# Optimization experiments

Measured on AMD Instinct MI355X. Metric: run time of the kernel, lower is better.

## Reference

```python
import jax, jax.numpy as jnp
import numpy as np

# ---- constants matching init_kwargs ----
ALPHA = 1.0
SCALING = 12.0
RESP_INDEX = (0, 1, 2, 3)
N_TARGETS = len(RESP_INDEX)
NDAYS = 250  # number of distinct date ids; with N=2M and 250 ids all are present
N = 2_000_000
N_RESP = 5


def setup_inputs() -> dict:
    key = jax.random.key(0)
    k1, k2, k3, k4 = jax.random.split(key, 4)
    inputs = jax.random.normal(k1, (N, N_RESP), dtype=jnp.float32)
    targets = jax.random.normal(k2, (N, N_RESP), dtype=jnp.float32)
    weights = jax.random.uniform(k3, (N,), dtype=jnp.float32)
    date = jax.random.randint(k4, (N,), 0, NDAYS, dtype=jnp.int64)
    return {"inputs": inputs, "targets": targets, "weights": weights, "date": date}


def reference(inputs, targets, weights, date):
    # slice resp columns (resp_index is not None and len < 5)
    idx = jnp.asarray(RESP_INDEX)
    x = jax.nn.sigmoid(SCALING * inputs[..., idx])   # [N, 4]
    t = targets[..., idx]                            # [N, 4]

    # faithful to torch: inputs/targets flattened sample-major, while
    # weights/date are repeat-tiled (resp-major) -- same pairing as original.
    x = x.reshape(-1)                 # [4N], sample-major
    t = t.reshape(-1)                 # [4N], sample-major
    w = jnp.tile(weights, N_TARGETS)  # [4N], tiled
    d = jnp.tile(date, N_TARGETS)     # [4N], tiled

    # per-day grouped sum -> single-pass segment reduction
    Pi = jax.ops.segment_sum(w * t * x, d, num_segments=NDAYS)  # [NDAYS]

    sumPi = Pi.sum()
    # normalize == 'mean'
    loss = -ALPHA * sumPi * jnp.maximum(sumPi, 0.0) / jnp.sum(Pi * Pi) / NDAYS
    return loss
```

## Files before the change

### kernel.cpp

```cpp
#include <hip/hip_runtime.h>

#define NDAYS 250
#define NRESP 5
#define SCALING 12.0f
#define NB 1024
#define T1 256
#define T2 1024
#define CHUNK 4

__global__ __launch_bounds__(T1) void pi_kernel(
    const float* __restrict__ inputs, const float* __restrict__ targets,
    const float* __restrict__ weights, const int* __restrict__ date,
    float* __restrict__ part, int n) {
    __shared__ float sPi[NDAYS];
    for (int i = threadIdx.x; i < NDAYS; i += T1) sPi[i] = 0.0f;
    __syncthreads();

    const int nq = n >> 2;
    const long qstep = (long)nq * NRESP;
    const long stride = (long)gridDim.x * T1;
    for (long m = (long)blockIdx.x * T1 + threadIdx.x; m < n; m += stride) {
        const int j = (int)(m & 3);
        const long base = (m >> 2) * NRESP + j;
        float acc = 0.0f;
        #pragma unroll
        for (int q = 0; q < 4; ++q) {
            const long idx = base + q * qstep;
            const float e = __expf(-SCALING * inputs[idx]);
            const float x = __builtin_amdgcn_rcpf(1.0f + e);
            acc += targets[idx] * x;
        }
        acc *= weights[m];
        const unsigned d = (unsigned)date[m];
        if (d < NDAYS) atomicAdd(&sPi[d], acc);
    }

    __syncthreads();
    float* row = part + (size_t)blockIdx.x * NDAYS;
    for (int i = threadIdx.x; i < NDAYS; i += T1) row[i] = sPi[i];
}

__global__ __launch_bounds__(T2) void finish_kernel(const float* __restrict__ part,
                                                    float* __restrict__ out) {
    __shared__ float red[CHUNK][256];
    __shared__ float ws_s[4], ws_q[4];
    const int t = threadIdx.x;
    const int d = t & 255;
    const int c = t >> 8;
    const int rows = NB / CHUNK;

    float acc = 0.0f;
    if (d < NDAYS) {
        const float* p = part + (size_t)c * rows * NDAYS + d;
        #pragma unroll 8
        for (int r = 0; r < rows; ++r) acc += p[(size_t)r * NDAYS];
    }
    red[c][d] = acc;
    __syncthreads();

    float s = 0.0f, q = 0.0f;
    if (t < 256) {
        const float p4 = red[0][t] + red[1][t] + red[2][t] + red[3][t];
        s = p4;
        q = p4 * p4;
    }
    #pragma unroll
    for (int off = 32; off > 0; off >>= 1) {
        s += __shfl_down(s, off);
        q += __shfl_down(q, off);
    }
    if (t < 256 && (t & 63) == 0) {
        ws_s[t >> 6] = s;
        ws_q[t >> 6] = q;
    }
    __syncthreads();
    if (t == 0) {
        const float sumPi = ws_s[0] + ws_s[1] + ws_s[2] + ws_s[3];
        const float sumPi2 = ws_q[0] + ws_q[1] + ws_q[2] + ws_q[3];
        out[0] = -1.0f * sumPi * fmaxf(sumPi, 0.0f) / sumPi2 / (float)NDAYS;
    }
}

extern "C" void kernel_launch(void* const* d_in, const int* in_sizes, int n_in,
                              void* d_out, int out_size, void* d_ws, size_t ws_size,
                              hipStream_t stream) {
    const float* inputs  = (const float*)d_in[0];
    const float* targets = (const float*)d_in[1];
    const float* weights = (const float*)d_in[2];
    const int*   date    = (const int*)d_in[3];
    float* out  = (float*)d_out;
    float* part = (float*)d_ws;

    const int n = in_sizes[2];

    pi_kernel<<<NB, T1, 0, stream>>>(inputs, targets, weights, date, part, n);
    finish_kernel<<<1, T2, 0, stream>>>(part, out);
}
```

Before: 125.8 us.

## Vectorize loads by processing 4 contiguous samples per thread with float4

Each thread now handles a group of 4 consecutive samples, loading the 20 contiguous input and target floats as five float4 vectors and the matching 16 weights and dates as float4/int4 loads. Previously each thread did four strided scalar gathers across the 5-column layout, so the new pattern is meant to cut memory transactions and use full-width loads. The cost is 16 shared-memory atomics per thread instead of one pre-summed atomic, which raises LDS contention. The bounds check on date is also dropped. Block and grid sizes are changed to 512x512.

```diff
diff --git a/kernel.cpp b/kernel.cpp
--- a/kernel.cpp
+++ b/kernel.cpp
@@ -1,12 +1,14 @@
 #include <hip/hip_runtime.h>
 
 #define NDAYS 250
-#define NRESP 5
 #define SCALING 12.0f
-#define NB 1024
-#define T1 256
+#define NB 512
+#define T1 512
 #define T2 1024
 #define CHUNK 4
+
+typedef float f4 __attribute__((ext_vector_type(4)));
+typedef int   i4 __attribute__((ext_vector_type(4)));
 
 __global__ __launch_bounds__(T1) void pi_kernel(
     const float* __restrict__ inputs, const float* __restrict__ targets,
@@ -16,23 +18,42 @@
     for (int i = threadIdx.x; i < NDAYS; i += T1) sPi[i] = 0.0f;
     __syncthreads();
 
-    const int nq = n >> 2;
-    const long qstep = (long)nq * NRESP;
+    const int ng = n >> 2;
     const long stride = (long)gridDim.x * T1;
-    for (long m = (long)blockIdx.x * T1 + threadIdx.x; m < n; m += stride) {
-        const int j = (int)(m & 3);
-        const long base = (m >> 2) * NRESP + j;
-        float acc = 0.0f;
+    for (long g = (long)blockIdx.x * T1 + threadIdx.x; g < ng; g += stride) {
+        long m = g << 4;
+        if (m >= n) m -= n;
+        if (m >= n) m -= n;
+        if (m >= n) m -= n;
+        const float* ip = inputs + g * 20;
+        const float* tp = targets + g * 20;
+        f4 in5[5], tg5[5];
         #pragma unroll
-        for (int q = 0; q < 4; ++q) {
-            const long idx = base + q * qstep;
-            const float e = __expf(-SCALING * inputs[idx]);
-            const float x = __builtin_amdgcn_rcpf(1.0f + e);
-            acc += targets[idx] * x;
+        for (int e = 0; e < 5; ++e) {
+            in5[e] = *(const f4*)(ip + 4 * e);
+            tg5[e] = *(const f4*)(tp + 4 * e);
         }
-        acc *= weights[m];
-        const unsigned d = (unsigned)date[m];
-        if (d < NDAYS) atomicAdd(&sPi[d], acc);
+        f4 w4[4]; i4 d4[4];
+        #pragma unroll
+        for (int e = 0; e < 4; ++e) {
+            w4[e] = *(const f4*)(weights + m + 4 * e);
+            d4[e] = *(const i4*)(date + m + 4 * e);
+        }
+        const float* in_f = (const float*)in5;
+        const float* tg_f = (const float*)tg5;
+        const float* w_f  = (const float*)w4;
+        const int*   d_i  = (const int*)d4;
+        #pragma unroll
+        for (int r = 0; r < 4; ++r) {
+            #pragma unroll
+            for (int j = 0; j < 4; ++j) {
+                const float xin = in_f[5 * r + j];
+                const float e1 = __expf(-SCALING * xin);
+                const float sg = __builtin_amdgcn_rcpf(1.0f + e1);
+                const float p = tg_f[5 * r + j] * sg * w_f[4 * r + j];
+                atomicAdd(&sPi[d_i[4 * r + j]], p);
+            }
+        }
     }
 
     __syncthreads();
```

Result: slower. 149.7 us (+19.0%).
